# Performance work log

Measured on AMD Instinct MI355X. Metric: run time of the kernel, lower is better.

Reference implementation:

```python
import jax, jax.numpy as jnp
import numpy as np

B, T, E = 2, 2048, 1024
NEXP, TOPK, INTER = 8, 2, 1408


def setup_inputs() -> dict:
    key = jax.random.key(0)
    ks = jax.random.split(key, 5)
    s = 0.02
    return {
        "x": jax.random.normal(ks[0], (B, T, E), dtype=jnp.float32),
        "gate_w": jax.random.normal(ks[1], (NEXP, E), dtype=jnp.float32) * s,
        "wg": jax.random.normal(ks[2], (NEXP, INTER, E), dtype=jnp.float32) * s,
        "wu": jax.random.normal(ks[3], (NEXP, INTER, E), dtype=jnp.float32) * s,
        "wd": jax.random.normal(ks[4], (NEXP, E, INTER), dtype=jnp.float32) * s,
    }


def reference(x, gate_w, wg, wu, wd):
    # Router: scores [B,T,NEXP], topk softmax over selected experts only
    scores = jnp.einsum("btd,ed->bte", x, gate_w)
    topk_scores, topk_idx = jax.lax.top_k(scores, TOPK)  # [B,T,K]
    topk_probs = jax.nn.softmax(topk_scores, axis=-1)
    # Scatter back to dense gating probs [B,T,NEXP] (topk indices are unique)
    onehot = jax.nn.one_hot(topk_idx, NEXP, dtype=x.dtype)  # [B,T,K,NEXP]
    gating = jnp.sum(onehot * topk_probs[..., None], axis=-2)  # [B,T,NEXP]
    # Dense compute-all-experts (faithful to the original module)
    g = jnp.einsum("btd,eid->btei", x, wg)  # [B,T,NEXP,INTER]
    u = jnp.einsum("btd,eid->btei", x, wu)
    h = jax.nn.silu(g) * u
    expert_out = jnp.einsum("btei,edi->bted", h, wd)  # [B,T,NEXP,E]
    y = jnp.sum(gating[..., None] * expert_out, axis=-2)  # [B,T,E]
    return y
```

## Files before the change

### kernel.cpp

```cpp
#include <hip/hip_runtime.h>
#include <hip/hip_bf16.h>
#include <stdint.h>

typedef __hip_bfloat16 bf16;
typedef __attribute__((ext_vector_type(8))) short short8;
typedef __attribute__((ext_vector_type(4))) float f32x4;

#define NTOK  4096
#define EDIM  1024
#define NEXPT 8
#define INTERD 1408
#define MAXP  4096
#define WELEM (NEXPT * INTERD * EDIM)

#define GL16(g, l) __builtin_amdgcn_global_load_lds( \
    (const __attribute__((address_space(1))) unsigned int*)(g), \
    (__attribute__((address_space(3))) unsigned int*)(l), 16, 0, 0)

#define WAIT_VM(n)   asm volatile("s_waitcnt vmcnt(" #n ")" ::: "memory")
#define BAR()        __builtin_amdgcn_s_barrier()
#define PRIO(n)      __builtin_amdgcn_s_setprio(n)

__global__ __launch_bounds__(256) void prep_kernel(const float* __restrict__ wg, bf16* __restrict__ wgb,
                                                   const float* __restrict__ wu, bf16* __restrict__ wub,
                                                   const float* __restrict__ wd, bf16* __restrict__ wdb,
                                                   const float* __restrict__ x,
                                                   const float* __restrict__ gw,
                                                   bf16* __restrict__ xb,
                                                   int* __restrict__ sel,
                                                   float* __restrict__ tprob) {
    int b = blockIdx.x;
    if (b < 3072) {
        const float* src; bf16* dst;
        if (b < 1024)      { src = wg; dst = wgb; }
        else if (b < 2048) { src = wu; dst = wub; b -= 1024; }
        else               { src = wd; dst = wdb; b -= 2048; }
        int i = (b * 256 + threadIdx.x) * 4;
        int stride = 1024 * 256 * 4;
        for (; i < WELEM; i += stride) {
            float4 v = *(const float4*)(src + i);
            ushort4 o; bf16 t;
            t = __float2bfloat16(v.x); o.x = *(unsigned short*)&t;
            t = __float2bfloat16(v.y); o.y = *(unsigned short*)&t;
            t = __float2bfloat16(v.z); o.z = *(unsigned short*)&t;
            t = __float2bfloat16(v.w); o.w = *(unsigned short*)&t;
            *(ushort4*)(dst + i) = o;
        }
        return;
    }
    int t = (b - 3072) * 4 + (threadIdx.x >> 6);
    int lane = threadIdx.x & 63;
    const float* xr = x + (size_t)t * EDIM;
    float xv[16];
#pragma unroll
    for (int j = 0; j < 4; j++) {
        float4 v = *(const float4*)(xr + lane * 16 + j * 4);
        xv[4 * j] = v.x; xv[4 * j + 1] = v.y; xv[4 * j + 2] = v.z; xv[4 * j + 3] = v.w;
    }
    bf16* xbr = xb + (size_t)t * EDIM;
#pragma unroll
    for (int j = 0; j < 4; j++) {
        ushort4 o; bf16 c;
        c = __float2bfloat16(xv[4 * j]);     o.x = *(unsigned short*)&c;
        c = __float2bfloat16(xv[4 * j + 1]); o.y = *(unsigned short*)&c;
        c = __float2bfloat16(xv[4 * j + 2]); o.z = *(unsigned short*)&c;
        c = __float2bfloat16(xv[4 * j + 3]); o.w = *(unsigned short*)&c;
        *(ushort4*)(xbr + lane * 16 + j * 4) = o;
    }
    double acc[NEXPT];
#pragma unroll
    for (int e = 0; e < NEXPT; e++) acc[e] = 0.0;
#pragma unroll
    for (int e = 0; e < NEXPT; e++) {
        const float* gr = gw + e * EDIM + lane * 16;
#pragma unroll
        for (int j = 0; j < 16; j++) acc[e] += (double)xv[j] * (double)gr[j];
    }
#pragma unroll
    for (int off = 32; off >= 1; off >>= 1) {
#pragma unroll
        for (int e = 0; e < NEXPT; e++) acc[e] += __shfl_xor(acc[e], off, 64);
    }
    if (lane == 0) {
        int e0 = 0; double s0 = acc[0];
        for (int e = 1; e < NEXPT; e++) if (acc[e] > s0) { s0 = acc[e]; e0 = e; }
        int e1 = -1; double s1 = -1e300;
        for (int e = 0; e < NEXPT; e++) if (e != e0 && acc[e] > s1) { s1 = acc[e]; e1 = e; }
        float z = __expf((float)(s1 - s0));
        float p0 = 1.f / (1.f + z);
        sel[t] = e0 | (e1 << 8);
        tprob[2 * t] = p0;
        tprob[2 * t + 1] = 1.f - p0;
    }
}

__global__ __launch_bounds__(512) void bucket_kernel(const int* __restrict__ sel,
                                                     const float* __restrict__ tprob,
                                                     int* __restrict__ counts,
                                                     int* __restrict__ offsets,
                                                     int* __restrict__ ptok,
                                                     float* __restrict__ pprob,
                                                     int* __restrict__ wq1,
                                                     int* __restrict__ wq2) {
    __shared__ int scnt[NEXPT];
    int w = threadIdx.x >> 6;
    int lane = threadIdx.x & 63;
    unsigned long long ltmask = (lane == 63) ? ~0ull >> 1 : (1ull << lane) - 1;
    int base = 0;
    for (int t0 = 0; t0 < NTOK; t0 += 64) {
        int t = t0 + lane;
        int s = sel[t];
        int e0 = s & 0xff, e1 = (s >> 8) & 0xff;
        unsigned long long m0 = __ballot(e0 == w);
        if (e0 == w) {
            int pos = base + __popcll(m0 & ltmask);
            ptok[w * MAXP + pos] = t;
            pprob[w * MAXP + pos] = tprob[2 * t];
        }
        base += __popcll(m0);
        unsigned long long m1 = __ballot(e1 == w);
        if (e1 == w) {
            int pos = base + __popcll(m1 & ltmask);
            ptok[w * MAXP + pos] = t;
            pprob[w * MAXP + pos] = tprob[2 * t + 1];
        }
        base += __popcll(m1);
    }
    if (lane == 0) scnt[w] = base;
    __syncthreads();
    if (threadIdx.x < NEXPT) {
        int off = 0;
        for (int e = 0; e < (int)threadIdx.x; e++) off += scnt[e];
        counts[threadIdx.x] = scnt[threadIdx.x];
        offsets[threadIdx.x] = off;
        wq1[threadIdx.x * 32] = 0;
        wq2[threadIdx.x * 32] = 0;
    }
}

__global__ __launch_bounds__(512, 4) void gemm1_kernel(const bf16* __restrict__ xb,
                                                       const bf16* __restrict__ wgb,
                                                       const bf16* __restrict__ wub,
                                                       bf16* __restrict__ hout,
                                                       const int* __restrict__ counts,
                                                       const int* __restrict__ offsets,
                                                       const int* __restrict__ ptok,
                                                       const float* __restrict__ pprob,
                                                       int* __restrict__ wq1) {
    int eown = blockIdx.x & 7;

    __shared__ __align__(16) bf16 smem[3 * 12288];
    __shared__ int s_wi;

    int tid  = threadIdx.x;
    int lane = tid & 63;
    int wid  = tid >> 6;
    int wm   = wid >> 2;
    int wn   = wid & 3;

    int srow = tid >> 2;
    int qs   = (((tid & 3) ^ ((srow >> 1) & 3)) * 8);
    int l15  = lane & 15;
    int l4   = lane >> 4;

    int offA[4], offG[2];
#pragma unroll
    for (int m = 0; m < 4; m++) {
        int r = wm * 64 + m * 16 + l15;
        offA[m] = r * 32 + ((l4 ^ ((r >> 1) & 3)) * 8);
    }
#pragma unroll
    for (int n = 0; n < 2; n++) {
        int r = wn * 32 + n * 16 + l15;
        offG[n] = r * 32 + ((l4 ^ ((r >> 1) & 3)) * 8);
    }

    for (int ei = 0; ei < NEXPT; ++ei) {
        int e = (eown + ei) & 7;
        int cnt = counts[e];
        int mtiles = (cnt + 127) >> 7;
        int tiles = mtiles * (INTERD / 128);
        int hbase = offsets[e];

        for (;;) {
            if (tid == 0) s_wi = atomicAdd(&wq1[e * 32], 1);
            __syncthreads();
            int wi = s_wi;
            __syncthreads();
            if (wi >= tiles) break;
            int mt = wi % mtiles;
            int nt = wi / mtiles;
            int m0 = mt * 128;
            int n0 = nt * 128;

            WAIT_VM(0);
            const bf16* gA = xb + (size_t)ptok[e * MAXP + min(m0 + srow, cnt - 1)] * EDIM + qs;
            const bf16* gG = wgb + ((size_t)e * INTERD + n0 + srow) * EDIM + qs;
            const bf16* gU = wub + ((size_t)e * INTERD + n0 + srow) * EDIM + qs;

            f32x4 accg[4][2], accu[4][2];
#pragma unroll
            for (int m = 0; m < 4; m++)
#pragma unroll
                for (int n = 0; n < 2; n++) {
                    accg[m][n] = (f32x4){0.f, 0.f, 0.f, 0.f};
                    accu[m][n] = (f32x4){0.f, 0.f, 0.f, 0.f};
                }

#define SB1(t) (smem + ((t) % 3) * 12288)
#define G1_STAGE(t) do { bf16* sb_ = SB1(t); int ko_ = (t) * 32; \
            GL16(gA + ko_, sb_ + wid * 512); \
            GL16(gG + ko_, sb_ + 4096 + wid * 512); \
            GL16(gU + ko_, sb_ + 8192 + wid * 512); } while (0)

            G1_STAGE(0); G1_STAGE(1);

            for (int t = 0; t < 32; ++t) {
                if (t < 30)       { G1_STAGE(t + 2); WAIT_VM(6); }
                else if (t == 30) { WAIT_VM(3); }
                else              { WAIT_VM(0); }
                BAR();
                const bf16* sb = SB1(t);
                short8 a_[4], gf[2], uf[2];
#pragma unroll
                for (int m = 0; m < 4; m++) a_[m] = *(const short8*)&sb[offA[m]];
#pragma unroll
                for (int n = 0; n < 2; n++) {
                    gf[n] = *(const short8*)&sb[4096 + offG[n]];
                    uf[n] = *(const short8*)&sb[8192 + offG[n]];
                }
                PRIO(1);
#pragma unroll
                for (int m = 0; m < 4; m++)
#pragma unroll
                    for (int n = 0; n < 2; n++) {
                        accg[m][n] = __builtin_amdgcn_mfma_f32_16x16x32_bf16(a_[m], gf[n], accg[m][n], 0, 0, 0);
                        accu[m][n] = __builtin_amdgcn_mfma_f32_16x16x32_bf16(a_[m], uf[n], accu[m][n], 0, 0, 0);
                    }
                PRIO(0);
                BAR();
            }
#undef SB1
#undef G1_STAGE

#pragma unroll
            for (int m = 0; m < 4; m++)
#pragma unroll
                for (int n = 0; n < 2; n++)
#pragma unroll
                    for (int r = 0; r < 4; r++) {
                        int pos = m0 + wm * 64 + m * 16 + l4 * 4 + r;
                        if (pos < cnt) {
                            int col = n0 + wn * 32 + n * 16 + l15;
                            float p = pprob[e * MAXP + pos];
                            float gv = accg[m][n][r];
                            float uv = accu[m][n][r];
                            float hv = (gv / (1.f + __expf(-gv))) * uv * p;
                            hout[(size_t)(hbase + pos) * INTERD + col] = __float2bfloat16(hv);
                        }
                    }
        }
    }
}

__global__ __launch_bounds__(256, 2) void gemm2_kernel(const bf16* __restrict__ h,
                                                       const bf16* __restrict__ wdb,
                                                       float* __restrict__ y,
                                                       const int* __restrict__ counts,
                                                       const int* __restrict__ offsets,
                                                       const int* __restrict__ ptok,
                                                       int* __restrict__ wq2) {
    int eown = blockIdx.x & 7;

    __shared__ __align__(16) bf16 smem[3 * 8192];
    __shared__ int s_wi;

    int tid  = threadIdx.x;
    int lane = tid & 63;
    int wid  = tid >> 6;
    int wm   = wid >> 1;
    int wn   = wid & 1;

    int srow = tid >> 2;
    int qs   = (((tid & 3) ^ ((srow >> 1) & 3)) * 8);
    int l15  = lane & 15;
    int l4   = lane >> 4;

    int offA[4], offB[4];
#pragma unroll
    for (int m = 0; m < 4; m++) {
        int r = wm * 64 + m * 16 + l15;
        offA[m] = r * 32 + ((l4 ^ ((r >> 1) & 3)) * 8);
    }
#pragma unroll
    for (int n = 0; n < 4; n++) {
        int r = wn * 64 + n * 16 + l15;
        offB[n] = 4096 + r * 32 + ((l4 ^ ((r >> 1) & 3)) * 8);
    }

    for (int ei = 0; ei < NEXPT; ++ei) {
        int e = (eown + ei) & 7;
        int cnt = counts[e];
        int mtiles = (cnt + 127) >> 7;
        int tiles = mtiles * (EDIM / 128);
        int hbase = offsets[e];

        for (;;) {
            if (tid == 0) s_wi = atomicAdd(&wq2[e * 32], 1);
            __syncthreads();
            int wi = s_wi;
            __syncthreads();
            if (wi >= tiles) break;
            int mt = wi % mtiles;
            int nt = wi / mtiles;
            int m0 = mt * 128;
            int n0 = nt * 128;

            WAIT_VM(0);
            const bf16* gA0 = h + (size_t)(hbase + min(m0 + srow,      cnt - 1)) * INTERD + qs;
            const bf16* gA1 = h + (size_t)(hbase + min(m0 + 64 + srow, cnt - 1)) * INTERD + qs;
            const bf16* gB0 = wdb + ((size_t)e * EDIM + n0 + srow) * INTERD + qs;
            const bf16* gB1 = wdb + ((size_t)e * EDIM + n0 + 64 + srow) * INTERD + qs;

            f32x4 acc[4][4];
#pragma unroll
            for (int m = 0; m < 4; m++)
#pragma unroll
                for (int n = 0; n < 4; n++) acc[m][n] = (f32x4){0.f, 0.f, 0.f, 0.f};

#define SB2(t) (smem + ((t) % 3) * 8192)
#define G2_STAGE(t) do { bf16* sb_ = SB2(t); int ko_ = (t) * 32; \
            GL16(gA0 + ko_, sb_ + wid * 512); \
            GL16(gA1 + ko_, sb_ + 2048 + wid * 512); \
            GL16(gB0 + ko_, sb_ + 4096 + wid * 512); \
            GL16(gB1 + ko_, sb_ + 6144 + wid * 512); } while (0)

            G2_STAGE(0); G2_STAGE(1);

            for (int t = 0; t < 44; ++t) {
                if (t < 42)       { G2_STAGE(t + 2); WAIT_VM(8); }
                else if (t == 42) { WAIT_VM(4); }
                else              { WAIT_VM(0); }
                BAR();
                const bf16* sb = SB2(t);
                short8 a_[4], b_[4];
#pragma unroll
                for (int m = 0; m < 4; m++) a_[m] = *(const short8*)&sb[offA[m]];
#pragma unroll
                for (int n = 0; n < 4; n++) b_[n] = *(const short8*)&sb[offB[n]];
                PRIO(1);
#pragma unroll
                for (int m = 0; m < 4; m++)
#pragma unroll
                    for (int n = 0; n < 4; n++)
                        acc[m][n] = __builtin_amdgcn_mfma_f32_16x16x32_bf16(a_[m], b_[n], acc[m][n], 0, 0, 0);
                PRIO(0);
                BAR();
            }
#undef SB2
#undef G2_STAGE

#pragma unroll
            for (int m = 0; m < 4; m++) {
                int pos = m0 + wm * 64 + m * 16 + l4 * 4;
                int tok[4];
#pragma unroll
                for (int r = 0; r < 4; r++)
                    tok[r] = (pos + r < cnt) ? ptok[e * MAXP + pos + r] : -1;
#pragma unroll
                for (int n = 0; n < 4; n++) {
                    int col = n0 + wn * 64 + n * 16 + l15;
#pragma unroll
                    for (int r = 0; r < 4; r++)
                        if (tok[r] >= 0)
                            atomicAdd(&y[(size_t)tok[r] * EDIM + col], acc[m][n][r]);
                }
            }
        }
    }
}

extern "C" void kernel_launch(void* const* d_in, const int* in_sizes, int n_in,
                              void* d_out, int out_size, void* d_ws, size_t ws_size,
                              hipStream_t stream) {
    const float* x      = (const float*)d_in[0];
    const float* gate_w = (const float*)d_in[1];
    const float* wg     = (const float*)d_in[2];
    const float* wu     = (const float*)d_in[3];
    const float* wd     = (const float*)d_in[4];
    float* y = (float*)d_out;

    char* ws = (char*)d_ws;
    constexpr size_t SZ_XB = (size_t)NTOK * EDIM * 2;
    constexpr size_t SZ_W  = (size_t)WELEM * 2;
    constexpr size_t SZ_H  = (size_t)NTOK * 2 * INTERD * 2;
    bf16* xb  = (bf16*)ws;
    bf16* wgb = (bf16*)(ws + SZ_XB);
    bf16* wub = (bf16*)(ws + SZ_XB + SZ_W);
    bf16* wdb = (bf16*)(ws + SZ_XB + 2 * SZ_W);
    bf16* h   = (bf16*)(ws + SZ_XB + 3 * SZ_W);
    char* meta = ws + SZ_XB + 3 * SZ_W + SZ_H;
    int*   counts  = (int*)meta;
    int*   offsets = (int*)(meta + 256);
    int*   ptok    = (int*)(meta + 512);
    float* pprob   = (float*)(meta + 512 + (size_t)NEXPT * MAXP * 4);
    char*  meta2   = meta + 512 + (size_t)NEXPT * MAXP * 8;
    int*   wq1     = (int*)meta2;
    int*   wq2     = (int*)(meta2 + 1024);
    int*   sel     = (int*)(meta2 + 2048);
    float* tprob   = (float*)(meta2 + 2048 + (size_t)NTOK * 4);

    hipMemsetAsync(d_out, 0, (size_t)out_size * 4, stream);

    prep_kernel<<<3072 + NTOK / 4, 256, 0, stream>>>(wg, wgb, wu, wub, wd, wdb,
                                                     x, gate_w, xb, sel, tprob);
    bucket_kernel<<<1, 512, 0, stream>>>(sel, tprob, counts, offsets, ptok, pprob,
                                         wq1, wq2);

    gemm1_kernel<<<512, 512, 0, stream>>>(
        xb, wgb, wub, h, counts, offsets, ptok, pprob, wq1);
    gemm2_kernel<<<512, 256, 0, stream>>>(
        h, wdb, y, counts, offsets, ptok, wq2);
}
```

Baseline: 249.8 us.

## Restructure gemm2 to 512 threads with BK=64 double-buffered tiles

```diff
diff --git a/kernel.cpp b/kernel.cpp
--- a/kernel.cpp
+++ b/kernel.cpp
@@ -263,7 +263,7 @@
     }
 }
 
-__global__ __launch_bounds__(256, 2) void gemm2_kernel(const bf16* __restrict__ h,
+__global__ __launch_bounds__(512, 4) void gemm2_kernel(const bf16* __restrict__ h,
                                                        const bf16* __restrict__ wdb,
                                                        float* __restrict__ y,
                                                        const int* __restrict__ counts,
@@ -272,30 +272,34 @@
                                                        int* __restrict__ wq2) {
     int eown = blockIdx.x & 7;
 
-    __shared__ __align__(16) bf16 smem[3 * 8192];
+    __shared__ __align__(16) bf16 smem[2 * 16384];
     __shared__ int s_wi;
 
     int tid  = threadIdx.x;
     int lane = tid & 63;
     int wid  = tid >> 6;
-    int wm   = wid >> 1;
-    int wn   = wid & 1;
-
-    int srow = tid >> 2;
-    int qs   = (((tid & 3) ^ ((srow >> 1) & 3)) * 8);
+    int wm   = wid >> 2;
+    int wn   = wid & 3;
+
+    int srow = tid >> 3;
+    int qs   = (((tid & 7) ^ (srow & 7)) * 8);
     int l15  = lane & 15;
     int l4   = lane >> 4;
 
-    int offA[4], offB[4];
+    int offA[4][2], offB[2][2];
 #pragma unroll
     for (int m = 0; m < 4; m++) {
         int r = wm * 64 + m * 16 + l15;
-        offA[m] = r * 32 + ((l4 ^ ((r >> 1) & 3)) * 8);
-    }
-#pragma unroll
-    for (int n = 0; n < 4; n++) {
-        int r = wn * 64 + n * 16 + l15;
-        offB[n] = 4096 + r * 32 + ((l4 ^ ((r >> 1) & 3)) * 8);
+#pragma unroll
+        for (int kh = 0; kh < 2; kh++)
+            offA[m][kh] = r * 64 + (((kh * 4 + l4) ^ (r & 7)) * 8);
+    }
+#pragma unroll
+    for (int n = 0; n < 2; n++) {
+        int r = wn * 32 + n * 16 + l15;
+#pragma unroll
+        for (int kh = 0; kh < 2; kh++)
+            offB[n][kh] = 8192 + r * 64 + (((kh * 4 + l4) ^ (r & 7)) * 8);
     }
 
     for (int ei = 0; ei < NEXPT; ++ei) {
@@ -322,38 +326,46 @@
             const bf16* gB0 = wdb + ((size_t)e * EDIM + n0 + srow) * INTERD + qs;
             const bf16* gB1 = wdb + ((size_t)e * EDIM + n0 + 64 + srow) * INTERD + qs;
 
-            f32x4 acc[4][4];
+            f32x4 acc[4][2];
 #pragma unroll
             for (int m = 0; m < 4; m++)
 #pragma unroll
-                for (int n = 0; n < 4; n++) acc[m][n] = (f32x4){0.f, 0.f, 0.f, 0.f};
-
-#define SB2(t) (smem + ((t) % 3) * 8192)
-#define G2_STAGE(t) do { bf16* sb_ = SB2(t); int ko_ = (t) * 32; \
+                for (int n = 0; n < 2; n++) acc[m][n] = (f32x4){0.f, 0.f, 0.f, 0.f};
+
+#define SB2(t) (smem + ((t) & 1) * 16384)
+#define G2_STAGE(t) do { bf16* sb_ = SB2(t); int ko_ = (t) * 64; \
             GL16(gA0 + ko_, sb_ + wid * 512); \
-            GL16(gA1 + ko_, sb_ + 2048 + wid * 512); \
-            GL16(gB0 + ko_, sb_ + 4096 + wid * 512); \
-            GL16(gB1 + ko_, sb_ + 6144 + wid * 512); } while (0)
-
-            G2_STAGE(0); G2_STAGE(1);
-
-            for (int t = 0; t < 44; ++t) {
-                if (t < 42)       { G2_STAGE(t + 2); WAIT_VM(8); }
-                else if (t == 42) { WAIT_VM(4); }
-                else              { WAIT_VM(0); }
+            GL16(gA1 + ko_, sb_ + 4096 + wid * 512); \
+            GL16(gB0 + ko_, sb_ + 8192 + wid * 512); \
+            GL16(gB1 + ko_, sb_ + 12288 + wid * 512); } while (0)
+
+            G2_STAGE(0);
+
+            for (int t = 0; t < 22; ++t) {
+                if (t < 21) { G2_STAGE(t + 1); WAIT_VM(4); }
+                else        { WAIT_VM(0); }
                 BAR();
                 const bf16* sb = SB2(t);
-                short8 a_[4], b_[4];
-#pragma unroll
-                for (int m = 0; m < 4; m++) a_[m] = *(const short8*)&sb[offA[m]];
-#pragma unroll
-                for (int n = 0; n < 4; n++) b_[n] = *(const short8*)&sb[offB[n]];
+                short8 a_[4][2], b_[2][2];
+#pragma unroll
+                for (int m = 0; m < 4; m++)
+#pragma unroll
+                    for (int kh = 0; kh < 2; kh++)
+                        a_[m][kh] = *(const short8*)&sb[offA[m][kh]];
+#pragma unroll
+                for (int n = 0; n < 2; n++)
+#pragma unroll
+                    for (int kh = 0; kh < 2; kh++)
+                        b_[n][kh] = *(const short8*)&sb[offB[n][kh]];
                 PRIO(1);
 #pragma unroll
                 for (int m = 0; m < 4; m++)
 #pragma unroll
-                    for (int n = 0; n < 4; n++)
-                        acc[m][n] = __builtin_amdgcn_mfma_f32_16x16x32_bf16(a_[m], b_[n], acc[m][n], 0, 0, 0);
+                    for (int n = 0; n < 2; n++)
+#pragma unroll
+                        for (int kh = 0; kh < 2; kh++)
+                            acc[m][n] = __builtin_amdgcn_mfma_f32_16x16x32_bf16(
+                                a_[m][kh], b_[n][kh], acc[m][n], 0, 0, 0);
                 PRIO(0);
                 BAR();
             }
@@ -368,8 +380,8 @@
                 for (int r = 0; r < 4; r++)
                     tok[r] = (pos + r < cnt) ? ptok[e * MAXP + pos + r] : -1;
 #pragma unroll
-                for (int n = 0; n < 4; n++) {
-                    int col = n0 + wn * 64 + n * 16 + l15;
+                for (int n = 0; n < 2; n++) {
+                    int col = n0 + wn * 32 + n * 16 + l15;
 #pragma unroll
                     for (int r = 0; r < 4; r++)
                         if (tok[r] >= 0)
@@ -419,6 +431,6 @@
 
     gemm1_kernel<<<512, 512, 0, stream>>>(
         xb, wgb, wub, h, counts, offsets, ptok, pprob, wq1);
-    gemm2_kernel<<<512, 256, 0, stream>>>(
+    gemm2_kernel<<<512, 512, 0, stream>>>(
         h, wdb, y, counts, offsets, ptok, wq2);
 }
```

Measured after the change: 239.8 us. 1.04x faster.
